# Optimization experiments

Hardware: AMD Instinct MI355X
Metric: run time of the kernel (lower is better)

Reference implementation:

```python
import jax, jax.numpy as jnp
import numpy as np

DEPTH = 5  # init kwarg


def setup_inputs() -> dict:
    key = jax.random.key(0)
    ks = jax.random.split(key, 10)
    n_atoms, n_bonds, hidden, n_mols = 80000, 160001, 448, 4000
    ATOM_DIM, BOND_DIM = 38, 11
    inp = {
        "fatoms": jax.random.normal(ks[0], (n_atoms, ATOM_DIM), jnp.float32),
        "fbonds": jax.random.normal(ks[1], (n_bonds, ATOM_DIM + BOND_DIM), jnp.float32),
        "W_i": jax.random.normal(ks[2], (ATOM_DIM + BOND_DIM, hidden), jnp.float32) * 0.1,
        "W_h": jax.random.normal(ks[3], (hidden, hidden), jnp.float32) * 0.05,
        "W_o": jax.random.normal(ks[4], (ATOM_DIM + hidden, hidden), jnp.float32) * 0.05,
        "b_o": jax.random.normal(ks[5], (hidden,), jnp.float32),
        "agraph": jax.random.randint(ks[6], (n_atoms, 6), 0, n_bonds, jnp.int64),
        "bgraph": jax.random.randint(ks[7], (n_bonds, 6), 0, n_bonds, jnp.int64),
        "mol_idx": jnp.sort(jax.random.randint(ks[8], (n_atoms,), 0, n_mols, jnp.int64)),
        "n_mols": n_mols,
    }
    return inp


def reference(fatoms, fbonds, W_i, W_h, W_o, b_o, agraph, bgraph, mol_idx, n_mols):
    # binput: [n_bonds, hidden]
    binput = fbonds @ W_i
    message = jax.nn.relu(binput)
    for _ in range(DEPTH - 1):
        # padded-neighbor gather-sum over MAX_NB=6, then linear + relu
        nei = jnp.take(message, bgraph, axis=0).sum(axis=1)  # [n_bonds, hidden]
        message = jax.nn.relu(binput + nei @ W_h)
    # atom readout
    nei = jnp.take(message, agraph, axis=0).sum(axis=1)  # [n_atoms, hidden]
    ainput = jnp.concatenate([fatoms, nei], axis=1)
    atom_hiddens = jax.nn.relu(ainput @ W_o + b_o)
    # per-molecule mean pooling (scope -> segment ids)
    sums = jax.ops.segment_sum(atom_hiddens, mol_idx, num_segments=n_mols)
    counts = jax.ops.segment_sum(jnp.ones((atom_hiddens.shape[0],), atom_hiddens.dtype), mol_idx, num_segments=n_mols)
    return sums / jnp.maximum(counts, 1.0)[:, None]
```

## Files before the change

### kernel.cpp

```cpp
#include <hip/hip_runtime.h>

#define HIDDEN 448

typedef __attribute__((ext_vector_type(8))) short short8;
typedef __attribute__((ext_vector_type(4))) float f32x4;

__device__ __forceinline__ unsigned short f2bf(float f) {
    unsigned int u = __float_as_uint(f);
    u = (u + 0x7fffu + ((u >> 16) & 1u)) >> 16;
    return (unsigned short)u;
}
__device__ __forceinline__ float bf2f(unsigned short h) {
    return __uint_as_float(((unsigned int)h) << 16);
}
__device__ __forceinline__ unsigned int cvt_pk_bf16(float a, float b) {
    unsigned int r;
    asm("v_cvt_pk_bf16_f32 %0, %1, %2" : "=v"(r) : "v"(a), "v"(b));
    return r;
}
__device__ __forceinline__ void async16(void* lds, const void* g) {
    __builtin_amdgcn_global_load_lds(
        (const __attribute__((address_space(1))) unsigned int*)g,
        (__attribute__((address_space(3))) unsigned int*)lds, 16, 0, 0);
}

__global__ __launch_bounds__(256) void prep_wcat_kernel(
    const float* __restrict__ Wtop, int Ktop, const float* __restrict__ Wbot,
    unsigned short* __restrict__ out)
{
    const int idx = blockIdx.x * 256 + threadIdx.x;
    if (idx >= 448 * 512) return;
    const int n = idx >> 9, k = idx & 511;
    float v = 0.0f;
    if (k < Ktop) v = Wtop[k * HIDDEN + n];
    else if (k >= 64) v = Wbot[(k - 64) * HIDDEN + n];
    out[(size_t)n * 512 + (k ^ (((n >> 1) & 3) << 3))] = f2bf(v);
}

__global__ __launch_bounds__(256) void prep_apad_kernel(
    const float* __restrict__ A, int K, unsigned short* __restrict__ out,
    int Mreal, int total)
{
    const int idx = blockIdx.x * 256 + threadIdx.x;
    if (idx >= total) return;
    const int row = idx >> 6, k = idx & 63;
    const float v = (row < Mreal && k < K) ? A[(size_t)row * K + k] : 0.0f;
    out[(size_t)row * 64 + (k ^ (((row >> 1) & 3) << 3))] = f2bf(v);
}

template<int GRAPH, int OUTQ>
__global__ __launch_bounds__(512, 4) void gemm_mfma_kernel(
    const unsigned short* __restrict__ Apad,
    const unsigned char* __restrict__ Xq,
    const float* __restrict__ Xs,
    const int* __restrict__ graph,
    const unsigned short* __restrict__ BT,
    const float* __restrict__ bias,
    unsigned char* __restrict__ outq,
    float* __restrict__ outs,
    const int* __restrict__ molv,
    float* __restrict__ dout,
    int M, int nsteps)
{
    __shared__ __align__(16) unsigned char smem[37888];
    unsigned short* As = (unsigned short*)smem;
    unsigned short* Bs = (unsigned short*)(smem + 8192);
    float* rmaxbuf = (float*)(smem + 36864);

    const int tid = threadIdx.x, lane = tid & 63, wv = tid >> 6;
    const int row0 = blockIdx.x * 64;
    const int wrow = (wv & 1) * 32;
    const int wcol = (wv >> 1) * 112;
    const int rr = lane & 15, ch = lane >> 4;
    const int lrow = lane >> 2, lq = lane & 3;

    const int arow = tid >> 3, asub = tid & 7;
    const int ahh = asub >> 2, ac = asub & 3;
    const int awaddr = arow * 64 + ahh * 32 + ((ac ^ ((arow >> 1) & 3)) << 3);

    int goff[6]; float gscl[6]; uint2 pf[6];
    if (GRAPH) {
        const int grow = row0 + arow;
        const bool ok = grow < M;
        #pragma unroll
        for (int j = 0; j < 6; ++j) {
            const int gj = ok ? graph[(size_t)grow * 6 + j] : 0;
            goff[j] = gj * 448;
            gscl[j] = ok ? Xs[gj] : 0.0f;
        }
    }

    f32x4 acc[2][7] = {};

    for (int s = 0; s < nsteps; ++s) {
        if (GRAPH && s >= 2 && !(s & 1)) {
            float a0 = 0, a1 = 0, a2 = 0, a3 = 0, a4 = 0, a5 = 0, a6 = 0, a7 = 0;
            #pragma unroll
            for (int j = 0; j < 6; ++j) {
                const uint2 b = pf[j];
                const float sc = gscl[j];
                a0 += (float)(b.x & 255u) * sc;
                a1 += (float)((b.x >> 8) & 255u) * sc;
                a2 += (float)((b.x >> 16) & 255u) * sc;
                a3 += (float)(b.x >> 24) * sc;
                a4 += (float)(b.y & 255u) * sc;
                a5 += (float)((b.y >> 8) & 255u) * sc;
                a6 += (float)((b.y >> 16) & 255u) * sc;
                a7 += (float)(b.y >> 24) * sc;
            }
            uint4 w;
            w.x = cvt_pk_bf16(a0, a1);
            w.y = cvt_pk_bf16(a2, a3);
            w.z = cvt_pk_bf16(a4, a5);
            w.w = cvt_pk_bf16(a6, a7);
            *(uint4*)&As[awaddr] = w;
        }
        #pragma unroll
        for (int i = 0; i < 4; ++i) {
            const int t = wv + 8 * i;
            if (t < 28)
                async16(Bs + t * 512 + lane * 8,
                        BT + (size_t)(t * 16 + lrow) * 512 + s * 32 + lq * 8);
        }
        if (s == 0)
            async16(As + wv * 512 + lane * 8,
                    Apad + (size_t)(row0 + wv * 8) * 64 + lane * 8);
        __syncthreads();

        if (GRAPH && !(s & 1) && s <= 12) {
            const int pb = (s >> 1) * 64;
            #pragma unroll
            for (int j = 0; j < 6; ++j)
                pf[j] = *(const uint2*)(Xq + goff[j] + pb + asub * 8);
        }

        const int hoff = (s & 1) * 32;
        short8 av[2], bv[7];
        #pragma unroll
        for (int m = 0; m < 2; ++m) {
            const int r = wrow + m * 16 + rr;
            av[m] = *(const short8*)&As[r * 64 + hoff + ((ch ^ ((r >> 1) & 3)) << 3)];
        }
        #pragma unroll
        for (int n = 0; n < 7; ++n) {
            const int cl = wcol + n * 16 + rr;
            bv[n] = *(const short8*)&Bs[cl * 32 + ((ch ^ ((cl >> 1) & 3)) << 3)];
        }
        #pragma unroll
        for (int n = 0; n < 7; ++n)
            #pragma unroll
            for (int m = 0; m < 2; ++m)
                acc[m][n] = __builtin_amdgcn_mfma_f32_16x16x32_bf16(
                    av[m], bv[n], acc[m][n], 0, 0, 0);

        __syncthreads();
    }

    const int r4 = ch << 2;

    if (OUTQ) {
        float rpm[2][4];
        #pragma unroll
        for (int m = 0; m < 2; ++m)
            #pragma unroll
            for (int j = 0; j < 4; ++j) {
                float mx = 0.0f;
                #pragma unroll
                for (int n = 0; n < 7; ++n) mx = fmaxf(mx, acc[m][n][j]);
                rpm[m][j] = mx;
            }
        #pragma unroll
        for (int off = 1; off < 16; off <<= 1)
            #pragma unroll
            for (int m = 0; m < 2; ++m)
                #pragma unroll
                for (int j = 0; j < 4; ++j)
                    rpm[m][j] = fmaxf(rpm[m][j], __shfl_xor(rpm[m][j], off));
        if (rr == 0)
            #pragma unroll
            for (int m = 0; m < 2; ++m)
                #pragma unroll
                for (int j = 0; j < 4; ++j)
                    rmaxbuf[(wrow + m * 16 + r4 + j) * 4 + (wv >> 1)] = rpm[m][j];
        __syncthreads();
        float inv[2][4];
        #pragma unroll
        for (int m = 0; m < 2; ++m)
            #pragma unroll
            for (int j = 0; j < 4; ++j) {
                const int rl = wrow + m * 16 + r4 + j;
                const float mx = fmaxf(fmaxf(rmaxbuf[rl * 4 + 0], rmaxbuf[rl * 4 + 1]),
                                       fmaxf(rmaxbuf[rl * 4 + 2], rmaxbuf[rl * 4 + 3]));
                inv[m][j] = (mx > 0.0f) ? (255.0f / mx) : 0.0f;
                if (wv < 2 && rr == 0 && row0 + rl < M)
                    outs[row0 + rl] = mx * (1.0f / 255.0f);
            }
        __syncthreads();
        unsigned char* q8 = smem;
        #pragma unroll
        for (int m = 0; m < 2; ++m)
            #pragma unroll
            for (int j = 0; j < 4; ++j) {
                const int rl = wrow + m * 16 + r4 + j;
                #pragma unroll
                for (int n = 0; n < 7; ++n) {
                    const float v = fmaxf(acc[m][n][j], 0.0f);
                    q8[rl * 448 + wcol + n * 16 + rr] =
                        (unsigned char)__float2uint_rn(fminf(v * inv[m][j], 255.0f));
                }
            }
        __syncthreads();
        #pragma unroll
        for (int i = 0; i < 4; ++i) {
            const int u = tid + 512 * i;
            if (u < 1792 && row0 + u / 28 < M)
                ((uint4*)(outq + (size_t)row0 * 448))[u] = ((const uint4*)q8)[u];
        }
    } else {
        int mols[2][4];
        #pragma unroll
        for (int m = 0; m < 2; ++m)
            #pragma unroll
            for (int j = 0; j < 4; ++j) {
                const int row = row0 + wrow + m * 16 + r4 + j;
                mols[m][j] = (row < M) ? molv[row] : -1;
            }
        #pragma unroll
        for (int n = 0; n < 7; ++n) {
            const int col = wcol + n * 16 + rr;
            const float bsv = bias ? bias[col] : 0.0f;
            #pragma unroll
            for (int m = 0; m < 2; ++m) {
                int curmol = -1;
                float rs = 0.0f;
                #pragma unroll
                for (int j = 0; j < 4; ++j) {
                    if (mols[m][j] >= 0) {
                        const float v = fmaxf(acc[m][n][j] + bsv, 0.0f);
                        if (mols[m][j] != curmol) {
                            if (curmol >= 0)
                                atomicAdd(dout + (size_t)curmol * HIDDEN + col, rs);
                            curmol = mols[m][j];
                            rs = v;
                        } else {
                            rs += v;
                        }
                    }
                }
                if (curmol >= 0)
                    atomicAdd(dout + (size_t)curmol * HIDDEN + col, rs);
            }
        }
    }
}

__global__ void norm_kernel(float* __restrict__ out,
                            const int* __restrict__ mol_idx, int n_atoms)
{
    const int m = blockIdx.x;
    const int c = threadIdx.x;
    int l = 0, r = n_atoms;
    while (l < r) { const int mid = (l + r) >> 1; if (mol_idx[mid] < m) l = mid + 1; else r = mid; }
    const int start = l;
    r = n_atoms;
    while (l < r) { const int mid = (l + r) >> 1; if (mol_idx[mid] < m + 1) l = mid + 1; else r = mid; }
    out[(size_t)m * HIDDEN + c] /= fmaxf((float)(l - start), 1.0f);
}

__global__ __launch_bounds__(256) void fill_kernel(float* __restrict__ out, int n, float val)
{
    const int i = blockIdx.x * 256 + threadIdx.x;
    if (i < n) out[i] = val;
}

extern "C" void kernel_launch(void* const* d_in, const int* in_sizes, int n_in,
                              void* d_out, int out_size, void* d_ws, size_t ws_size,
                              hipStream_t stream)
{
    const float* fatoms = (const float*)d_in[0];
    const float* fbonds = (const float*)d_in[1];
    const float* W_i    = (const float*)d_in[2];
    const float* W_h    = (const float*)d_in[3];
    const float* W_o    = (const float*)d_in[4];
    const float* b_o    = (const float*)d_in[5];
    const int*   agraph = (const int*)d_in[6];
    const int*   bgraph = (const int*)d_in[7];
    const int*   mol_idx= (const int*)d_in[8];

    const int n_atoms = in_sizes[0] / 38;
    const int n_bonds = in_sizes[1] / 49;
    const int n_mols  = out_size / HIDDEN;

    const int Mb_b = (n_bonds + 63) & ~63;
    const int Mb_a = (n_atoms + 63) & ~63;

    const size_t eW  = (size_t)448 * 512;
    const size_t eFb = (size_t)Mb_b * 64;
    const size_t eFa = (size_t)Mb_a * 64;
    const size_t eX  = (size_t)Mb_b * 448;

    const size_t need = 2 * eW * 2 + eFb * 2 + eFa * 2 +
                        2 * eX + 2 * (size_t)Mb_b * 4;

    const dim3 blk(256);

    if (ws_size >= need) {
        unsigned short* WhcatT  = (unsigned short*)d_ws;
        unsigned short* WocatT  = WhcatT + eW;
        unsigned short* fbondsP = WocatT + eW;
        unsigned short* fatomsP = fbondsP + eFb;
        unsigned char*  Xq0     = (unsigned char*)(fatomsP + eFa);
        unsigned char*  Xq1     = Xq0 + eX;
        float*          Xs0     = (float*)(Xq1 + eX);
        float*          Xs1     = Xs0 + Mb_b;

        hipMemsetAsync(d_out, 0, (size_t)out_size * sizeof(float), stream);

        const int wblocks = (448 * 512 + 255) / 256;
        hipLaunchKernelGGL(prep_wcat_kernel, dim3(wblocks), blk, 0, stream,
                           W_i, 49, W_h, WhcatT);
        hipLaunchKernelGGL(prep_wcat_kernel, dim3(wblocks), blk, 0, stream,
                           W_o, 38, W_o + 38 * HIDDEN, WocatT);
        hipLaunchKernelGGL(prep_apad_kernel, dim3(((int)eFb + 255) / 256), blk, 0, stream,
                           fbonds, 49, fbondsP, n_bonds, (int)eFb);
        hipLaunchKernelGGL(prep_apad_kernel, dim3(((int)eFa + 255) / 256), blk, 0, stream,
                           fatoms, 38, fatomsP, n_atoms, (int)eFa);

        const dim3 gB(Mb_b / 64), gA(Mb_a / 64), tpb(512);

        unsigned char* Xq[2] = {Xq0, Xq1};
        float*         Xs[2] = {Xs0, Xs1};

        hipLaunchKernelGGL((gemm_mfma_kernel<0, 1>), gB, tpb, 0, stream,
                           fbondsP, (const unsigned char*)nullptr, (const float*)nullptr,
                           (const int*)nullptr, WhcatT, (const float*)nullptr,
                           Xq[0], Xs[0], (const int*)nullptr, (float*)nullptr,
                           n_bonds, 2);
        int p = 0;
        for (int it = 0; it < 4; ++it) {
            hipLaunchKernelGGL((gemm_mfma_kernel<1, 1>), gB, tpb, 0, stream,
                               fbondsP, Xq[p], Xs[p], bgraph, WhcatT,
                               (const float*)nullptr,
                               Xq[p ^ 1], Xs[p ^ 1], (const int*)nullptr,
                               (float*)nullptr, n_bonds, 16);
            p ^= 1;
        }
        hipLaunchKernelGGL((gemm_mfma_kernel<1, 0>), gA, tpb, 0, stream,
                           fatomsP, Xq[p], Xs[p], agraph, WocatT, b_o,
                           (unsigned char*)nullptr, (float*)nullptr,
                           mol_idx, (float*)d_out, n_atoms, 16);
        hipLaunchKernelGGL(norm_kernel, dim3(n_mols), dim3(HIDDEN), 0, stream,
                           (float*)d_out, mol_idx, n_atoms);
    } else {
        const float val = -(float)((double)ws_size / (1024.0 * 1024.0));
        hipLaunchKernelGGL(fill_kernel, dim3((out_size + 255) / 256), blk, 0, stream,
                           (float*)d_out, out_size, val);
    }
}
```

Baseline: 882.3 us.

## Double-buffer gathered A tile and merge prep kernels into one launch

The gemm kernel now keeps two A-tile buffers in shared memory. The neighbor gather-sum for the next K-chunk is computed after the MFMAs of the current step and written into the other buffer, so the gather reduction overlaps with the matrix math instead of running before it. Neighbor prefetches move to odd steps, and the first chunk is loaded in the prologue. Separately, the four prep kernels are merged into a single launch to cut launch overhead. Shared memory per block grows from about 37 KB to 45 KB, which may lower occupancy.

```diff
diff --git a/kernel.cpp b/kernel.cpp
--- a/kernel.cpp
+++ b/kernel.cpp
@@ -24,28 +24,43 @@
         (__attribute__((address_space(3))) unsigned int*)lds, 16, 0, 0);
 }
 
-__global__ __launch_bounds__(256) void prep_wcat_kernel(
-    const float* __restrict__ Wtop, int Ktop, const float* __restrict__ Wbot,
-    unsigned short* __restrict__ out)
-{
-    const int idx = blockIdx.x * 256 + threadIdx.x;
-    if (idx >= 448 * 512) return;
-    const int n = idx >> 9, k = idx & 511;
-    float v = 0.0f;
-    if (k < Ktop) v = Wtop[k * HIDDEN + n];
-    else if (k >= 64) v = Wbot[(k - 64) * HIDDEN + n];
-    out[(size_t)n * 512 + (k ^ (((n >> 1) & 3) << 3))] = f2bf(v);
-}
-
-__global__ __launch_bounds__(256) void prep_apad_kernel(
-    const float* __restrict__ A, int K, unsigned short* __restrict__ out,
-    int Mreal, int total)
-{
-    const int idx = blockIdx.x * 256 + threadIdx.x;
-    if (idx >= total) return;
-    const int row = idx >> 6, k = idx & 63;
-    const float v = (row < Mreal && k < K) ? A[(size_t)row * K + k] : 0.0f;
-    out[(size_t)row * 64 + (k ^ (((row >> 1) & 3) << 3))] = f2bf(v);
+__global__ __launch_bounds__(256) void prep_all_kernel(
+    const float* __restrict__ W_i, const float* __restrict__ W_h,
+    const float* __restrict__ W_o,
+    const float* __restrict__ fbonds, const float* __restrict__ fatoms,
+    unsigned short* __restrict__ WhcatT, unsigned short* __restrict__ WocatT,
+    unsigned short* __restrict__ fbondsP, unsigned short* __restrict__ fatomsP,
+    int n_bonds, int n_atoms, int eFb, int eFa)
+{
+    const int eww = 448 * 512;
+    int idx = blockIdx.x * 256 + threadIdx.x;
+    if (idx < 2 * eww) {
+        const int seg = idx >= eww;
+        const int i = seg ? idx - eww : idx;
+        const int n = i >> 9, k = i & 511;
+        const float* Wtop = seg ? W_o : W_i;
+        const float* Wbot = seg ? (W_o + 38 * HIDDEN) : W_h;
+        const int Ktop = seg ? 38 : 49;
+        float v = 0.0f;
+        if (k < Ktop) v = Wtop[k * HIDDEN + n];
+        else if (k >= 64) v = Wbot[(k - 64) * HIDDEN + n];
+        unsigned short* out = seg ? WocatT : WhcatT;
+        out[(size_t)n * 512 + (k ^ (((n >> 1) & 3) << 3))] = f2bf(v);
+        return;
+    }
+    idx -= 2 * eww;
+    if (idx < eFb) {
+        const int row = idx >> 6, k = idx & 63;
+        const float v = (row < n_bonds && k < 49) ? fbonds[(size_t)row * 49 + k] : 0.0f;
+        fbondsP[(size_t)row * 64 + (k ^ (((row >> 1) & 3) << 3))] = f2bf(v);
+        return;
+    }
+    idx -= eFb;
+    if (idx < eFa) {
+        const int row = idx >> 6, k = idx & 63;
+        const float v = (row < n_atoms && k < 38) ? fatoms[(size_t)row * 38 + k] : 0.0f;
+        fatomsP[(size_t)row * 64 + (k ^ (((row >> 1) & 3) << 3))] = f2bf(v);
+    }
 }
 
 template<int GRAPH, int OUTQ>
@@ -62,10 +77,9 @@
     float* __restrict__ dout,
     int M, int nsteps)
 {
-    __shared__ __align__(16) unsigned char smem[37888];
-    unsigned short* As = (unsigned short*)smem;
-    unsigned short* Bs = (unsigned short*)(smem + 8192);
-    float* rmaxbuf = (float*)(smem + 36864);
+    __shared__ __align__(16) unsigned char smem[46080];
+    unsigned short* Bs = (unsigned short*)(smem + 16384);
+    float* rmaxbuf = (float*)(smem + 45056);
 
     const int tid = threadIdx.x, lane = tid & 63, wv = tid >> 6;
     const int row0 = blockIdx.x * 64;
@@ -88,12 +102,55 @@
             goff[j] = gj * 448;
             gscl[j] = ok ? Xs[gj] : 0.0f;
         }
+        #pragma unroll
+        for (int j = 0; j < 6; ++j)
+            pf[j] = *(const uint2*)(Xq + goff[j] + asub * 8);
     }
 
     f32x4 acc[2][7] = {};
 
     for (int s = 0; s < nsteps; ++s) {
-        if (GRAPH && s >= 2 && !(s & 1)) {
+        const int q = s >> 1;
+        #pragma unroll
+        for (int i = 0; i < 4; ++i) {
+            const int t = wv + 8 * i;
+            if (t < 28)
+                async16(Bs + t * 512 + lane * 8,
+                        BT + (size_t)(t * 16 + lrow) * 512 + s * 32 + lq * 8);
+        }
+        if (s == 0)
+            async16((unsigned short*)smem + wv * 512 + lane * 8,
+                    Apad + (size_t)(row0 + wv * 8) * 64 + lane * 8);
+        __syncthreads();
+
+        if (GRAPH && (s & 1) && s <= 11) {
+            const int pb = (q + 1) * 64;
+            #pragma unroll
+            for (int j = 0; j < 6; ++j)
+                pf[j] = *(const uint2*)(Xq + goff[j] + pb + asub * 8);
+        }
+
+        unsigned short* AsCur = (unsigned short*)(smem + (size_t)(q & 1) * 8192);
+        const int hoff = (s & 1) * 32;
+        short8 av[2], bv[7];
+        #pragma unroll
+        for (int m = 0; m < 2; ++m) {
+            const int r = wrow + m * 16 + rr;
+            av[m] = *(const short8*)&AsCur[r * 64 + hoff + ((ch ^ ((r >> 1) & 3)) << 3)];
+        }
+        #pragma unroll
+        for (int n = 0; n < 7; ++n) {
+            const int cl = wcol + n * 16 + rr;
+            bv[n] = *(const short8*)&Bs[cl * 32 + ((ch ^ ((cl >> 1) & 3)) << 3)];
+        }
+        #pragma unroll
+        for (int n = 0; n < 7; ++n)
+            #pragma unroll
+            for (int m = 0; m < 2; ++m)
+                acc[m][n] = __builtin_amdgcn_mfma_f32_16x16x32_bf16(
+                    av[m], bv[n], acc[m][n], 0, 0, 0);
+
+        if (GRAPH && !(s & 1) && s <= 12) {
             float a0 = 0, a1 = 0, a2 = 0, a3 = 0, a4 = 0, a5 = 0, a6 = 0, a7 = 0;
             #pragma unroll
             for (int j = 0; j < 6; ++j) {
@@ -113,45 +170,10 @@
             w.y = cvt_pk_bf16(a2, a3);
             w.z = cvt_pk_bf16(a4, a5);
             w.w = cvt_pk_bf16(a6, a7);
-            *(uint4*)&As[awaddr] = w;
-        }
-        #pragma unroll
-        for (int i = 0; i < 4; ++i) {
-            const int t = wv + 8 * i;
-            if (t < 28)
-                async16(Bs + t * 512 + lane * 8,
-                        BT + (size_t)(t * 16 + lrow) * 512 + s * 32 + lq * 8);
-        }
-        if (s == 0)
-            async16(As + wv * 512 + lane * 8,
-                    Apad + (size_t)(row0 + wv * 8) * 64 + lane * 8);
-        __syncthreads();
-
-        if (GRAPH && !(s & 1) && s <= 12) {
-            const int pb = (s >> 1) * 64;
-            #pragma unroll
-            for (int j = 0; j < 6; ++j)
-                pf[j] = *(const uint2*)(Xq + goff[j] + pb + asub * 8);
-        }
-
-        const int hoff = (s & 1) * 32;
-        short8 av[2], bv[7];
-        #pragma unroll
-        for (int m = 0; m < 2; ++m) {
-            const int r = wrow + m * 16 + rr;
-            av[m] = *(const short8*)&As[r * 64 + hoff + ((ch ^ ((r >> 1) & 3)) << 3)];
-        }
-        #pragma unroll
-        for (int n = 0; n < 7; ++n) {
-            const int cl = wcol + n * 16 + rr;
-            bv[n] = *(const short8*)&Bs[cl * 32 + ((ch ^ ((cl >> 1) & 3)) << 3)];
-        }
-        #pragma unroll
-        for (int n = 0; n < 7; ++n)
-            #pragma unroll
-            for (int m = 0; m < 2; ++m)
-                acc[m][n] = __builtin_amdgcn_mfma_f32_16x16x32_bf16(
-                    av[m], bv[n], acc[m][n], 0, 0, 0);
+            unsigned short* AsNxt =
+                (unsigned short*)(smem + (size_t)((q + 1) & 1) * 8192);
+            *(uint4*)&AsNxt[awaddr] = w;
+        }
 
         __syncthreads();
     }
@@ -316,15 +338,11 @@
 
         hipMemsetAsync(d_out, 0, (size_t)out_size * sizeof(float), stream);
 
-        const int wblocks = (448 * 512 + 255) / 256;
-        hipLaunchKernelGGL(prep_wcat_kernel, dim3(wblocks), blk, 0, stream,
-                           W_i, 49, W_h, WhcatT);
-        hipLaunchKernelGGL(prep_wcat_kernel, dim3(wblocks), blk, 0, stream,
-                           W_o, 38, W_o + 38 * HIDDEN, WocatT);
-        hipLaunchKernelGGL(prep_apad_kernel, dim3(((int)eFb + 255) / 256), blk, 0, stream,
-                           fbonds, 49, fbondsP, n_bonds, (int)eFb);
-        hipLaunchKernelGGL(prep_apad_kernel, dim3(((int)eFa + 255) / 256), blk, 0, stream,
-                           fatoms, 38, fatomsP, n_atoms, (int)eFa);
+        const int prep_total = 2 * (int)eW + (int)eFb + (int)eFa;
+        hipLaunchKernelGGL(prep_all_kernel, dim3((prep_total + 255) / 256), blk, 0, stream,
+                           W_i, W_h, W_o, fbonds, fatoms,
+                           WhcatT, WocatT, fbondsP, fatomsP,
+                           n_bonds, n_atoms, (int)eFb, (int)eFa);
 
         const dim3 gB(Mb_b / 64), gA(Mb_a / 64), tpb(512);
 
```

Result: no change. 890.4 us (+0.9%).
